# Performance work log

Measured on AMD Instinct MI355X. Metric: run time of the kernel, lower is better.

The kernel has to match this reference:

```python
import jax, jax.numpy as jnp
import numpy as np

B, N, M, C, G = 8, 1024, 20000, 80, 64
NMS_THR = 0.5
PULL_W = 1.0
PUSH_W = 1.0
EPS = 1e-6


def _rand_boxes(key, shape):
    k1, k2 = jax.random.split(key)
    xy = jax.random.uniform(k1, shape + (2,), minval=0.0, maxval=900.0)
    wh = jax.random.uniform(k2, shape + (2,), minval=8.0, maxval=120.0)
    return jnp.concatenate([xy, xy + wh], axis=-1).astype(jnp.float32)


def setup_inputs() -> dict:
    key = jax.random.key(0)
    ks = jax.random.split(key, 6)
    return {
        "pos_inds": jax.random.randint(ks[0], (B, N), 0, M, dtype=jnp.int32),
        "pos_gt_index": jax.random.randint(ks[1], (B, N), 0, G, dtype=jnp.int32),
        "gt_bboxes": _rand_boxes(ks[2], (B, G)),
        "bbox_preds": _rand_boxes(ks[3], (B, N)),
        "cls_scores": jax.random.uniform(ks[4], (B, M, C), dtype=jnp.float32),
        "gt_labels": jax.random.randint(ks[5], (B, G), 0, C, dtype=jnp.int32),
    }


def pairwise_iou(b1, b2):
    # legacy +1 convention, matching bbox_overlaps(mode='iou')
    lt = jnp.maximum(b1[:, None, :2], b2[None, :, :2])
    rb = jnp.minimum(b1[:, None, 2:], b2[None, :, 2:])
    wh = jnp.clip(rb - lt + 1.0, 0.0)
    ov = wh[..., 0] * wh[..., 1]
    a1 = (b1[:, 2] - b1[:, 0] + 1.0) * (b1[:, 3] - b1[:, 1] + 1.0)
    a2 = (b2[:, 2] - b2[:, 0] + 1.0) * (b2[:, 3] - b2[:, 1] + 1.0)
    return ov / (a1[:, None] + a2[None, :] - ov)


def nms_loss_single(boxes, scores, gt_index, gt_boxes):
    # boxes [N,4], scores [N], gt_index [N] int, gt_boxes [G,4]
    n = boxes.shape[0]
    g_n = gt_boxes.shape[0]
    # push_select=True: first operand of IoU is detached
    iou = pairwise_iou(jax.lax.stop_gradient(boxes), boxes)  # [N,N]
    gtiou = jax.lax.stop_gradient(pairwise_iou(gt_boxes, gt_boxes))  # [G,G]
    s_det = jax.lax.stop_gradient(scores)

    init = (jnp.ones((n,), bool), -jnp.ones((g_n,), jnp.int32),
            jnp.float32(0.0), jnp.float32(0.0), jnp.int32(0), jnp.int32(0))

    def step(carry, _):
        alive, seen, tpull, tpush, pcnt, qcnt = carry
        any_alive = jnp.any(alive)
        i = jnp.argmax(jnp.where(alive, s_det, -jnp.inf))  # pop highest score
        g = gt_index[i]
        prev = seen[g]
        has_seen = (prev >= 0) & any_alive
        # pull: pull_relax=True, use_score=True
        max_s_iou = jnp.maximum(iou[prev, i], EPS)
        pull = jnp.where(has_seen, -jnp.log(1.0 - NMS_THR + max_s_iou) * scores[i], 0.0)
        seen = jnp.where(any_alive & (prev < 0), seen.at[g].set(i.astype(jnp.int32)), seen)
        pcnt = pcnt + has_seen.astype(jnp.int32)
        alive = alive.at[i].set(False)
        remaining = jnp.any(alive)  # torch breaks (dropping this step's pull) if empty
        row = iou[i]
        overlap = alive & (row > NMS_THR)
        push_mask = overlap & (gt_index != g) & (row > gtiou[g, gt_index])
        n_push = jnp.sum(push_mask)
        # push: push_relax=False, use_score=True, scores NOT detached
        terms = -jnp.log(jnp.where(push_mask, 1.0 - row, 1.0)) * scores
        push = jnp.where(n_push > 0,
                         jnp.sum(jnp.where(push_mask, terms, 0.0)) / jnp.maximum(n_push, 1).astype(jnp.float32),
                         0.0)
        add = any_alive & remaining
        tpull = tpull + jnp.where(add, pull, 0.0)
        tpush = tpush + jnp.where(add, push, 0.0)
        qcnt = qcnt + jnp.where(add, n_push.astype(jnp.int32), 0)
        alive = alive & ~overlap
        return (alive, seen, tpull, tpush, pcnt, qcnt), None

    (alive, seen, tpull, tpush, pcnt, qcnt), _ = jax.lax.scan(step, init, None, length=n)
    pull = tpull / (pcnt.astype(jnp.float32) + EPS)
    push = tpush / (qcnt.astype(jnp.float32) + EPS)
    return push, pull


def reference(pos_inds, pos_gt_index, gt_bboxes, bbox_preds, cls_scores, gt_labels):
    labels = jnp.take_along_axis(gt_labels, pos_gt_index, axis=1)            # [B,N]
    sel = jnp.take_along_axis(cls_scores, pos_inds[..., None], axis=1)       # [B,N,C]
    scores = jnp.take_along_axis(sel, labels[..., None].astype(jnp.int32), axis=2)[..., 0]  # [B,N]
    push, pull = jax.vmap(nms_loss_single)(bbox_preds, scores, pos_gt_index, gt_bboxes)
    return jnp.stack([jnp.mean(push) * PUSH_W, jnp.mean(pull) * PULL_W])
```

## Files before the change

kernel.cpp:

```cpp
#include <hip/hip_runtime.h>
#include <math.h>

#define B_ 8
#define N_ 1024
#define M_ 20000
#define C_ 80
#define G_ 64
typedef unsigned long long ull;

#define WS_ELEM_OFF 0
#define WS_ADJ_OFF  262144

__device__ __forceinline__ float iou1(float ax, float ay, float az, float aw,
                                      float bx, float by, float bz, float bw) {
    float lx = fmaxf(ax, bx), ly = fmaxf(ay, by);
    float rx = fminf(az, bz), ry = fminf(aw, bw);
    float w = fmaxf(rx - lx + 1.0f, 0.0f), h = fmaxf(ry - ly + 1.0f, 0.0f);
    float ov = w * h;
    float a1 = (az - ax + 1.0f) * (aw - ay + 1.0f);
    float a2 = (bz - bx + 1.0f) * (bw - by + 1.0f);
    return ov / (a1 + a2 - ov);
}

__global__ __launch_bounds__(1024) void prep_kernel(
    const int* __restrict__ pos_inds, const int* __restrict__ pos_gt,
    const float* __restrict__ bbox_preds, const float* __restrict__ cls_scores,
    const int* __restrict__ gt_labels, float4* __restrict__ elemG,
    float* __restrict__ out) {
    const int b = blockIdx.x, t = threadIdx.x;
    __shared__ ull s_k2[2][N_];

    if (b == 0 && t == 0) { out[0] = 0.f; out[1] = 0.f; }

    int g0 = pos_gt[b * N_ + t];
    int lab = gt_labels[b * G_ + g0];
    int pi = pos_inds[b * N_ + t];
    float s = cls_scores[(size_t)b * (M_ * C_) + (size_t)pi * C_ + lab];
    ull key = ((ull)(~__float_as_uint(s)) << 32) | (unsigned)t;

    int pb = 0;
    for (unsigned k2 = 2; k2 <= N_; k2 <<= 1) {
        for (unsigned jj = k2 >> 1; jj; jj >>= 1) {
            ull other;
            if (jj >= 64) {
                s_k2[pb][t] = key;
                __syncthreads();
                other = s_k2[pb][t ^ jj];
                pb ^= 1;
            } else {
                int lo = __shfl_xor((int)(unsigned)key, (int)jj);
                int hi = __shfl_xor((int)(unsigned)(key >> 32), (int)jj);
                other = ((ull)(unsigned)hi << 32) | (unsigned)lo;
            }
            bool keep_min = (((t & jj) == 0) == ((t & k2) == 0));
            ull mn = key < other ? key : other;
            ull mx = key < other ? other : key;
            key = keep_min ? mn : mx;
        }
    }

    int j = (int)(unsigned)(key & 0xFFFFFFFFull);
    float ss = __uint_as_float(~(unsigned)(key >> 32));
    const float* bp = bbox_preds + (size_t)(b * N_ + j) * 4;
    float x0 = bp[0], y0 = bp[1], x1 = bp[2], y1 = bp[3];
    int g = pos_gt[b * N_ + j];
    float area = (x1 - x0 + 1.0f) * (y1 - y0 + 1.0f);
    elemG[(size_t)(b * N_ + t) * 2 + 0] = make_float4(x0, y0, x1, y1);
    elemG[(size_t)(b * N_ + t) * 2 + 1] = make_float4(__int_as_float(g), ss, area, 0.f);
}

__global__ __launch_bounds__(256) void adj_kernel(
    const float4* __restrict__ elemG, unsigned short* __restrict__ adjG) {
    const int b = blockIdx.y;
    const int r = blockIdx.x * 4 + (threadIdx.x >> 6);
    const int lane = threadIdx.x & 63;
    if ((lane >> 2) > (r >> 6)) return;
    float4 rA = elemG[(size_t)(b * N_ + r) * 2];
    float ax0 = rA.x, ay0 = rA.y;
    float az1 = rA.z + 1.0f, aw1 = rA.w + 1.0f;
    float a1 = (rA.z - rA.x + 1.0f) * (rA.w - rA.y + 1.0f);
    unsigned bits = 0;
#pragma unroll
    for (int u = 0; u < 16; ++u) {
        int cpos = lane * 16 + u;
        float4 cA = elemG[(size_t)(b * N_ + cpos) * 2];
        float lx = fmaxf(ax0, cA.x), ly = fmaxf(ay0, cA.y);
        float rx = fminf(az1, cA.z + 1.0f), ry = fminf(aw1, cA.w + 1.0f);
        float w = fmaxf(rx - lx, 0.0f), h = fmaxf(ry - ly, 0.0f);
        float I = w * h;
        float a2 = (cA.z - cA.x + 1.0f) * (cA.w - cA.y + 1.0f);
        bits |= (3.0f * I > a1 + a2) ? (1u << u) : 0u;
    }
    adjG[(size_t)(b * N_ + r) * 64 + lane] = (unsigned short)bits;
}

__global__ __launch_bounds__(1024) void sweep_loss_kernel(
    const float4* __restrict__ elemG, const unsigned short* __restrict__ adjG,
    const float* __restrict__ gt_bboxes, float* __restrict__ out) {
    const int b = blockIdx.x, t = threadIdx.x;
    const int wtop = t >> 6, lane = t & 63;

    __shared__ float4 s_box[N_];
    __shared__ float s_score[N_];
    __shared__ short s_g[N_];
    __shared__ ull s_S[16];
    __shared__ unsigned short s_step[N_];
    __shared__ unsigned short s_surv[N_];
    __shared__ float s_ts[N_];
    __shared__ int s_cnt[N_], s_kills[N_], s_first[G_];
    __shared__ int s_wpre[17];
    __shared__ float s_tpull, s_tpush;
    __shared__ int s_pcnt, s_qcnt;

    {
        float4 eA = elemG[(size_t)(b * N_ + t) * 2];
        float4 eB = elemG[(size_t)(b * N_ + t) * 2 + 1];
        s_box[t] = eA; s_score[t] = eB.y; s_g[t] = (short)__float_as_int(eB.x);
    }
    s_ts[t] = 0.f; s_cnt[t] = 0; s_kills[t] = 0; s_step[t] = 0xffff;
    if (t < 16) s_S[t] = 0ull;
    if (t < G_) s_first[t] = 0x7fffffff;
    if (t == 0) { s_tpull = 0.f; s_tpush = 0.f; s_pcnt = 0; s_qcnt = 0; }

    const ull* rowp = (const ull*)(adjG + (size_t)(b * N_ + t) * 64);
    ull rw[16];
#pragma unroll
    for (int c = 0; c < 16; ++c) rw[c] = (c <= wtop) ? rowp[c] : 0ull;

    __syncthreads();

    bool alive_f = true;
#pragma unroll
    for (int c = 0; c < 16; ++c) {
        if (wtop == c) {
            ull alive = __ballot(alive_f);
            ull Sc = 0ull;
            const ull below = (1ull << lane) - 1ull;
            const ull myearly = rw[c] & below;
            while (alive) {
                bool inU = ((alive >> lane) & 1ull) && ((myearly & alive) == 0ull);
                ull U = __ballot(inU);
                unsigned klo = inU ? (unsigned)rw[c] : 0u;
                unsigned khi = inU ? (unsigned)(rw[c] >> 32) : 0u;
#pragma unroll
                for (int off = 32; off; off >>= 1) {
                    klo |= (unsigned)__shfl_xor((int)klo, off);
                    khi |= (unsigned)__shfl_xor((int)khi, off);
                }
                ull kills = ((ull)khi << 32) | klo;
                Sc |= U;
                alive &= ~U;
                alive &= ~kills;
            }
            if (lane == 0) s_S[c] = Sc;
        }
        __syncthreads();
        if (wtop > c && alive_f && (rw[c] & s_S[c]) != 0ull) alive_f = false;
    }

    if (t < 16) s_wpre[t + 1] = __popcll(s_S[t]);
    __syncthreads();
    if (t == 0) { s_wpre[0] = 0; for (int w = 0; w < 16; ++w) s_wpre[w + 1] += s_wpre[w]; }
    __syncthreads();
    const int K = s_wpre[16];
    const ull sbit = 1ull << lane;
    const bool isS = (s_S[wtop] & sbit) != 0ull;
    int myrank = -1;
    if (isS) {
        myrank = s_wpre[wtop] + __popcll(s_S[wtop] & (sbit - 1ull));
        s_step[t] = (unsigned short)myrank;
        s_surv[myrank] = (unsigned short)t;
        atomicMin(&s_first[(int)s_g[t]], myrank);
    }
    __syncthreads();

    if (!isS) {
        int kp = -1;
#pragma unroll
        for (int w = 15; w >= 0; --w) {
            ull m = rw[w] & s_S[w];
            if (w == wtop) m &= (1ull << lane) - 1ull;
            if (m) kp = (w << 6) + (int)(__ffsll(m) - 1);
        }
        if (kp >= 0) {
            int q = s_step[kp];
            atomicAdd(&s_kills[q], 1);
            int gq = (int)s_g[kp], gj = (int)s_g[t];
            if (gq != gj) {
                float4 qa = s_box[kp], ja = s_box[t];
                float ov = iou1(qa.x, qa.y, qa.z, qa.w, ja.x, ja.y, ja.z, ja.w);
                const float* gbq = gt_bboxes + (size_t)(b * G_ + gq) * 4;
                const float* gbj = gt_bboxes + (size_t)(b * G_ + gj) * 4;
                float gov = iou1(gbq[0], gbq[1], gbq[2], gbq[3],
                                 gbj[0], gbj[1], gbj[2], gbj[3]);
                if (ov > gov) {
                    atomicAdd(&s_cnt[q], 1);
                    atomicAdd(&s_ts[q], -__logf(1.0f - ov) * s_score[t]);
                }
            }
        }
    }
    __syncthreads();

    if (isS) {
        int k = myrank, g = (int)s_g[t], f = s_first[g];
        if (f < k) {
            atomicAdd(&s_pcnt, 1);
            bool drop = (k == K - 1) && (s_kills[k] == 0);
            if (!drop) {
                float4 fA = s_box[s_surv[f]], kA = s_box[t];
                float ov = iou1(fA.x, fA.y, fA.z, fA.w, kA.x, kA.y, kA.z, kA.w);
                atomicAdd(&s_tpull, -__logf(0.5f + fmaxf(ov, 1e-6f)) * s_score[t]);
            }
        }
        if (s_cnt[k] > 0) {
            atomicAdd(&s_tpush, s_ts[k] / (float)s_cnt[k]);
            atomicAdd(&s_qcnt, s_cnt[k]);
        }
    }
    __syncthreads();

    if (t == 0) {
        atomicAdd(&out[0], (s_tpush / ((float)s_qcnt + 1e-6f)) * 0.125f);
        atomicAdd(&out[1], (s_tpull / ((float)s_pcnt + 1e-6f)) * 0.125f);
    }
}

extern "C" void kernel_launch(void* const* d_in, const int* in_sizes, int n_in,
                              void* d_out, int out_size, void* d_ws, size_t ws_size,
                              hipStream_t stream) {
    const int* pos_inds = (const int*)d_in[0];
    const int* pos_gt = (const int*)d_in[1];
    const float* gt_bboxes = (const float*)d_in[2];
    const float* bbox_preds = (const float*)d_in[3];
    const float* cls_scores = (const float*)d_in[4];
    const int* gt_labels = (const int*)d_in[5];
    float* out = (float*)d_out;

    float4* elemG = (float4*)((char*)d_ws + WS_ELEM_OFF);
    unsigned short* adjG = (unsigned short*)((char*)d_ws + WS_ADJ_OFF);

    prep_kernel<<<dim3(B_), dim3(1024), 0, stream>>>(
        pos_inds, pos_gt, bbox_preds, cls_scores, gt_labels, elemG, out);
    adj_kernel<<<dim3(256, B_), dim3(256), 0, stream>>>(elemG, adjG);
    sweep_loss_kernel<<<dim3(B_), dim3(1024), 0, stream>>>(elemG, adjG, gt_bboxes, out);
}
```

Before: 134.2 us.

## Split box/meta workspace, build adjacency words via ballot, simplify greedy sweep

Splits the per-element workspace into a dense float4 box array and a float2 metadata array, so the adjacency kernel reads contiguous, coalesced boxes. Each adjacency word is now produced by a wave-wide ballot over 64 columns and stored as a 64-bit word, with the loop bounded to the lower-triangle tiles instead of computing all columns and masking. The in-wave greedy sweep replaces the 12-shuffle OR reduction of kill masks with a second ballot that recomputes the alive set. GT boxes are staged in shared memory instead of being re-read from global memory. The data-dependent loop bound in the adjacency kernel gives waves unequal work, and the new alive-set rule depends on each row having its full mask of earlier neighbours.

```diff
diff --git a/kernel.cpp b/kernel.cpp
--- a/kernel.cpp
+++ b/kernel.cpp
@@ -8,7 +8,8 @@
 #define G_ 64
 typedef unsigned long long ull;
 
-#define WS_ELEM_OFF 0
+#define WS_BOX_OFF  0
+#define WS_META_OFF 131072
 #define WS_ADJ_OFF  262144
 
 __device__ __forceinline__ float iou1(float ax, float ay, float az, float aw,
@@ -25,8 +26,8 @@
 __global__ __launch_bounds__(1024) void prep_kernel(
     const int* __restrict__ pos_inds, const int* __restrict__ pos_gt,
     const float* __restrict__ bbox_preds, const float* __restrict__ cls_scores,
-    const int* __restrict__ gt_labels, float4* __restrict__ elemG,
-    float* __restrict__ out) {
+    const int* __restrict__ gt_labels, float4* __restrict__ boxesG,
+    float2* __restrict__ metaG, float* __restrict__ out) {
     const int b = blockIdx.x, t = threadIdx.x;
     __shared__ ull s_k2[2][N_];
 
@@ -64,45 +65,46 @@
     const float* bp = bbox_preds + (size_t)(b * N_ + j) * 4;
     float x0 = bp[0], y0 = bp[1], x1 = bp[2], y1 = bp[3];
     int g = pos_gt[b * N_ + j];
-    float area = (x1 - x0 + 1.0f) * (y1 - y0 + 1.0f);
-    elemG[(size_t)(b * N_ + t) * 2 + 0] = make_float4(x0, y0, x1, y1);
-    elemG[(size_t)(b * N_ + t) * 2 + 1] = make_float4(__int_as_float(g), ss, area, 0.f);
+    boxesG[b * N_ + t] = make_float4(x0, y0, x1, y1);
+    metaG[b * N_ + t] = make_float2(__int_as_float(g), ss);
 }
 
 __global__ __launch_bounds__(256) void adj_kernel(
-    const float4* __restrict__ elemG, unsigned short* __restrict__ adjG) {
+    const float4* __restrict__ boxesG, ull* __restrict__ adjG) {
     const int b = blockIdx.y;
     const int r = blockIdx.x * 4 + (threadIdx.x >> 6);
     const int lane = threadIdx.x & 63;
-    if ((lane >> 2) > (r >> 6)) return;
-    float4 rA = elemG[(size_t)(b * N_ + r) * 2];
+    const int wtop = r >> 6;
+    const float4* bb = boxesG + (size_t)b * N_;
+    float4 rA = bb[r];
     float ax0 = rA.x, ay0 = rA.y;
     float az1 = rA.z + 1.0f, aw1 = rA.w + 1.0f;
     float a1 = (rA.z - rA.x + 1.0f) * (rA.w - rA.y + 1.0f);
-    unsigned bits = 0;
-#pragma unroll
-    for (int u = 0; u < 16; ++u) {
-        int cpos = lane * 16 + u;
-        float4 cA = elemG[(size_t)(b * N_ + cpos) * 2];
+    ull myword = 0ull;
+    for (int u = 0; u <= wtop; ++u) {
+        float4 cA = bb[u * 64 + lane];
         float lx = fmaxf(ax0, cA.x), ly = fmaxf(ay0, cA.y);
         float rx = fminf(az1, cA.z + 1.0f), ry = fminf(aw1, cA.w + 1.0f);
         float w = fmaxf(rx - lx, 0.0f), h = fmaxf(ry - ly, 0.0f);
         float I = w * h;
         float a2 = (cA.z - cA.x + 1.0f) * (cA.w - cA.y + 1.0f);
-        bits |= (3.0f * I > a1 + a2) ? (1u << u) : 0u;
-    }
-    adjG[(size_t)(b * N_ + r) * 64 + lane] = (unsigned short)bits;
+        ull word = __ballot(3.0f * I > a1 + a2);
+        if (lane == u) myword = word;
+    }
+    if (lane <= wtop) adjG[(size_t)(b * N_ + r) * 16 + lane] = myword;
 }
 
 __global__ __launch_bounds__(1024) void sweep_loss_kernel(
-    const float4* __restrict__ elemG, const unsigned short* __restrict__ adjG,
-    const float* __restrict__ gt_bboxes, float* __restrict__ out) {
+    const float4* __restrict__ boxesG, const float2* __restrict__ metaG,
+    const ull* __restrict__ adjG, const float* __restrict__ gt_bboxes,
+    float* __restrict__ out) {
     const int b = blockIdx.x, t = threadIdx.x;
     const int wtop = t >> 6, lane = t & 63;
 
     __shared__ float4 s_box[N_];
     __shared__ float s_score[N_];
     __shared__ short s_g[N_];
+    __shared__ float4 s_gt[G_];
     __shared__ ull s_S[16];
     __shared__ unsigned short s_step[N_];
     __shared__ unsigned short s_surv[N_];
@@ -113,16 +115,17 @@
     __shared__ int s_pcnt, s_qcnt;
 
     {
-        float4 eA = elemG[(size_t)(b * N_ + t) * 2];
-        float4 eB = elemG[(size_t)(b * N_ + t) * 2 + 1];
-        s_box[t] = eA; s_score[t] = eB.y; s_g[t] = (short)__float_as_int(eB.x);
-    }
+        float4 bx = boxesG[b * N_ + t];
+        float2 mt = metaG[b * N_ + t];
+        s_box[t] = bx; s_score[t] = mt.y; s_g[t] = (short)__float_as_int(mt.x);
+    }
+    if (t < G_) s_gt[t] = ((const float4*)gt_bboxes)[b * G_ + t];
     s_ts[t] = 0.f; s_cnt[t] = 0; s_kills[t] = 0; s_step[t] = 0xffff;
     if (t < 16) s_S[t] = 0ull;
     if (t < G_) s_first[t] = 0x7fffffff;
     if (t == 0) { s_tpull = 0.f; s_tpush = 0.f; s_pcnt = 0; s_qcnt = 0; }
 
-    const ull* rowp = (const ull*)(adjG + (size_t)(b * N_ + t) * 64);
+    const ull* rowp = adjG + (size_t)(b * N_ + t) * 16;
     ull rw[16];
 #pragma unroll
     for (int c = 0; c < 16; ++c) rw[c] = (c <= wtop) ? rowp[c] : 0ull;
@@ -138,19 +141,11 @@
             const ull below = (1ull << lane) - 1ull;
             const ull myearly = rw[c] & below;
             while (alive) {
-                bool inU = ((alive >> lane) & 1ull) && ((myearly & alive) == 0ull);
+                bool me = (alive >> lane) & 1ull;
+                bool inU = me && ((myearly & alive) == 0ull);
                 ull U = __ballot(inU);
-                unsigned klo = inU ? (unsigned)rw[c] : 0u;
-                unsigned khi = inU ? (unsigned)(rw[c] >> 32) : 0u;
-#pragma unroll
-                for (int off = 32; off; off >>= 1) {
-                    klo |= (unsigned)__shfl_xor((int)klo, off);
-                    khi |= (unsigned)__shfl_xor((int)khi, off);
-                }
-                ull kills = ((ull)khi << 32) | klo;
                 Sc |= U;
-                alive &= ~U;
-                alive &= ~kills;
+                alive = __ballot(me && !inU && ((myearly & U) == 0ull));
             }
             if (lane == 0) s_S[c] = Sc;
         }
@@ -189,10 +184,9 @@
             if (gq != gj) {
                 float4 qa = s_box[kp], ja = s_box[t];
                 float ov = iou1(qa.x, qa.y, qa.z, qa.w, ja.x, ja.y, ja.z, ja.w);
-                const float* gbq = gt_bboxes + (size_t)(b * G_ + gq) * 4;
-                const float* gbj = gt_bboxes + (size_t)(b * G_ + gj) * 4;
-                float gov = iou1(gbq[0], gbq[1], gbq[2], gbq[3],
-                                 gbj[0], gbj[1], gbj[2], gbj[3]);
+                float4 gq4 = s_gt[gq], gj4 = s_gt[gj];
+                float gov = iou1(gq4.x, gq4.y, gq4.z, gq4.w,
+                                 gj4.x, gj4.y, gj4.z, gj4.w);
                 if (ov > gov) {
                     atomicAdd(&s_cnt[q], 1);
                     atomicAdd(&s_ts[q], -__logf(1.0f - ov) * s_score[t]);
@@ -237,11 +231,12 @@
     const int* gt_labels = (const int*)d_in[5];
     float* out = (float*)d_out;
 
-    float4* elemG = (float4*)((char*)d_ws + WS_ELEM_OFF);
-    unsigned short* adjG = (unsigned short*)((char*)d_ws + WS_ADJ_OFF);
+    float4* boxesG = (float4*)((char*)d_ws + WS_BOX_OFF);
+    float2* metaG = (float2*)((char*)d_ws + WS_META_OFF);
+    ull* adjG = (ull*)((char*)d_ws + WS_ADJ_OFF);
 
     prep_kernel<<<dim3(B_), dim3(1024), 0, stream>>>(
-        pos_inds, pos_gt, bbox_preds, cls_scores, gt_labels, elemG, out);
-    adj_kernel<<<dim3(256, B_), dim3(256), 0, stream>>>(elemG, adjG);
-    sweep_loss_kernel<<<dim3(B_), dim3(1024), 0, stream>>>(elemG, adjG, gt_bboxes, out);
-}
+        pos_inds, pos_gt, bbox_preds, cls_scores, gt_labels, boxesG, metaG, out);
+    adj_kernel<<<dim3(256, B_), dim3(256), 0, stream>>>(boxesG, adjG);
+    sweep_loss_kernel<<<dim3(B_), dim3(1024), 0, stream>>>(boxesG, metaG, adjG, gt_bboxes, out);
+}
```

Measured after the change: 125.3 us. 6.7% less time.
